# Optimization experiments

Hardware: AMD Instinct MI355X
Metric: run time of the kernel (lower is better)

## Reference

```python
import jax, jax.numpy as jnp
import numpy as np

B, N, C, H = 2, 2048, 1024, 16
HD = C // H  # head dim = 64


def setup_inputs() -> dict:
    key = jax.random.key(0)
    kq, kk, kv, km = jax.random.split(key, 4)
    q = jax.random.normal(kq, (B, N, C), dtype=jnp.float32)
    k = jax.random.normal(kk, (B, N, C), dtype=jnp.float32)
    v = jax.random.normal(kv, (B, N, C), dtype=jnp.float32)
    mask = jax.random.randint(km, (B, 1, N, N), 0, 2, dtype=jnp.int32)
    return {"q": q, "k": k, "v": v, "mask": mask}


def reference(q, k, v, mask):
    b, n, c = q.shape
    # (B, N, C) -> (B, H, N, HD)
    qh = q.reshape(b, n, H, HD).transpose(0, 2, 1, 3)
    kh = k.reshape(b, n, H, HD).transpose(0, 2, 1, 3)
    vh = v.reshape(b, n, H, HD).transpose(0, 2, 1, 3)
    scale = 1.0 / jnp.sqrt(jnp.float32(HD))
    # scores: (B, H, N, N)
    scores = jnp.einsum("bhqd,bhkd->bhqk", qh, kh) * scale
    scores = jnp.where(mask == 0, jnp.float32(-1e9), scores)
    probs = jax.nn.softmax(scores, axis=-1)
    atten = jnp.einsum("bhqk,bhkd->bhqd", probs, vh)
    # (B, H, N, HD) -> (B, N, C)
    return atten.transpose(0, 2, 1, 3).reshape(b, n, c)
```

## Files before the change

### kernel.cpp

```cpp
#include <hip/hip_runtime.h>
#include <hip/hip_bf16.h>

#define B_ 2
#define N_ 2048
#define C_ 1024
#define H_ 16
#define HD_ 64

#define KT 64
#define NT (N_ / KT)
#define TILE_E 4096
#define PSTR 72
#define NW 8
#define QB 128

#define NWM 4
#define QBM 64

typedef short s16x8 __attribute__((ext_vector_type(8)));
typedef short s16x4 __attribute__((ext_vector_type(4)));
typedef float f32x4 __attribute__((ext_vector_type(4)));

__device__ __forceinline__ ushort f2bf(float x) {
    __hip_bfloat16 h = __float2bfloat16(x);
    return *reinterpret_cast<ushort*>(&h);
}

__device__ __forceinline__ s16x8 cvt8(float4 a, float4 b) {
    union { s16x8 v; __hip_bfloat162 h[4]; } u;
    u.h[0] = __float22bfloat162_rn(float2{a.x, a.y});
    u.h[1] = __float22bfloat162_rn(float2{a.z, a.w});
    u.h[2] = __float22bfloat162_rn(float2{b.x, b.y});
    u.h[3] = __float22bfloat162_rn(float2{b.z, b.w});
    return u.v;
}

__device__ __forceinline__ void gll16(const void* g, void* l) {
    __builtin_amdgcn_global_load_lds(
        (const __attribute__((address_space(1))) unsigned*)g,
        (__attribute__((address_space(3))) unsigned*)l, 16, 0, 0);
}

__global__ __launch_bounds__(256)
void pack_mask(const int* __restrict__ M, unsigned long long* __restrict__ bits) {
    const int gw   = (blockIdx.x * 256 + threadIdx.x) >> 6;
    const int lane = threadIdx.x & 63;
#pragma unroll
    for (int it = 0; it < 16; ++it) {
        const size_t wi = (size_t)gw * 16 + it;
        unsigned long long bal = __ballot(M[wi * 64 + lane] != 0);
        if (lane == 0) bits[wi] = bal;
    }
}

__global__ __launch_bounds__(256)
void prepass(const int* __restrict__ M, const float* __restrict__ K,
             const float* __restrict__ V, unsigned long long* __restrict__ bits,
             ushort* __restrict__ Kw, ushort* __restrict__ Vw) {
    const int bid = blockIdx.x;
    const int tid = threadIdx.x;
    if (bid < 2048) {
        const int gw   = (bid * 256 + tid) >> 6;
        const int lane = tid & 63;
#pragma unroll
        for (int it = 0; it < 16; ++it) {
            const size_t wi = (size_t)gw * 16 + it;
            unsigned long long bal = __ballot(M[wi * 64 + lane] != 0);
            if (lane == 0) bits[wi] = bal;
        }
    } else if (bid < 4096) {
        const int gt = (bid - 2048) * 256 + tid;
        const int b  = gt >> 18;
        const int h  = (gt >> 14) & 15;
        const int n  = (gt >> 3) & 2047;
        const int db = gt & 7;
        const size_t src = (size_t)(b * N_ + n) * C_ + h * 64 + db * 8;
        float4 f0 = *(const float4*)(K + src);
        float4 f1 = *(const float4*)(K + src + 4);
        const int key = n & 63, kt = n >> 6;
        ushort* dst = Kw + (size_t)((b * H_ + h) * NT + kt) * TILE_E
                         + key * 64 + ((db ^ (key & 7)) * 8);
        *(s16x8*)dst = cvt8(f0, f1);
    } else {
        const int gt  = (bid - 4096) * 256 + tid;
        const int b   = gt >> 16;
        const int h   = (gt >> 12) & 15;
        const int kt  = (gt >> 7) & 31;
        const int kb4 = (gt >> 3) & 15;
        const int db  = gt & 7;
        const int key0 = kb4 * 4;
        float f[4][8];
#pragma unroll
        for (int i = 0; i < 4; ++i) {
            const size_t src = (size_t)(b * N_ + kt * 64 + key0 + i) * C_ + h * 64 + db * 8;
            *(float4*)&f[i][0] = *(const float4*)(V + src);
            *(float4*)&f[i][4] = *(const float4*)(V + src + 4);
        }
        ushort* tb = Vw + (size_t)((b * H_ + h) * NT + kt) * TILE_E;
#pragma unroll
        for (int j = 0; j < 8; ++j) {
            const int d = db * 8 + j;
            union { s16x4 v; __hip_bfloat162 h2[2]; } u;
            u.h2[0] = __float22bfloat162_rn(float2{f[0][j], f[1][j]});
            u.h2[1] = __float22bfloat162_rn(float2{f[2][j], f[3][j]});
            *(s16x4*)(tb + d * 64 + (((key0 >> 3) ^ (d & 7)) * 8) + (key0 & 7)) = u.v;
        }
    }
}

__global__ __launch_bounds__(256, 4)
void mha_fwd(const float* __restrict__ Q, const ushort* __restrict__ Kw,
             const ushort* __restrict__ Vw, const unsigned* __restrict__ bits,
             float* __restrict__ O) {
    __shared__ ushort Kl[2][TILE_E];
    __shared__ ushort Vt[2][TILE_E];
    __shared__ ushort Pl[NWM][16 * 64];

    const int sid = blockIdx.x;
    const int jj  = sid >> 3;
    const int hb  = ((sid & 7) << 2) | (jj & 3);
    const int qt  = jj >> 2;
    const int h   = hb & 15;
    const int b   = hb >> 4;

    const int tid  = threadIdx.x;
    const int w    = tid >> 6;
    const int lane = tid & 63;
    const int l16  = lane & 15;
    const int quad = lane >> 4;

    const size_t head_off = (size_t)b * N_ * C_ + (size_t)h * HD_;
    const int qb = qt * QBM + w * 16;

    const float qs = 0.125f * 1.44269504088896f;
    const size_t qoff = head_off + (size_t)(qb + l16) * C_ + quad * 8;
    float4 q0 = *(const float4*)(Q + qoff);
    float4 q1 = *(const float4*)(Q + qoff + 4);
    float4 q2 = *(const float4*)(Q + qoff + 32);
    float4 q3 = *(const float4*)(Q + qoff + 36);
    q0.x*=qs; q0.y*=qs; q0.z*=qs; q0.w*=qs;
    q1.x*=qs; q1.y*=qs; q1.z*=qs; q1.w*=qs;
    q2.x*=qs; q2.y*=qs; q2.z*=qs; q2.w*=qs;
    q3.x*=qs; q3.y*=qs; q3.z*=qs; q3.w*=qs;
    const s16x8 qa0 = cvt8(q0, q1);
    const s16x8 qa1 = cvt8(q2, q3);

    f32x4 acc[4];
#pragma unroll
    for (int c = 0; c < 4; ++c) acc[c] = f32x4{0.f, 0.f, 0.f, 0.f};
    float2 ls2 = {0.f, 0.f};

    const int fbase = l16 * 64 + ((quad ^ (l16 & 7)) * 8);
    const int prow  = l16 * 64;
    const int pswz  = (l16 & 7) << 1;

    const size_t tilebase = (size_t)((b * H_ + h) * NT) * TILE_E;
    const ushort* Kg = Kw + tilebase + (size_t)tid * 8;
    const ushort* Vg = Vw + tilebase + (size_t)tid * 8;

    const unsigned* mq = bits + ((size_t)b * N_ + qb + l16) * (N_ / 32);

    gll16(Kg,        &Kl[0][w * 512]);
    gll16(Kg + 2048, &Kl[0][w * 512 + 2048]);
    gll16(Vg,        &Vt[0][w * 512]);
    gll16(Vg + 2048, &Vt[0][w * 512 + 2048]);
    const ushort* Kg_pf = Kg + TILE_E;
    const ushort* Vg_pf = Vg + TILE_E;

    uint4 mw = *(const uint4*)mq;  mq += 4;

    for (int kt2 = 0; kt2 < NT; kt2 += 2) {
        const uint4 mw_nxt = *(const uint4*)mq;  mq += 4;
        const bool pf1 = (kt2 + 2 < NT);
#pragma unroll
        for (int u = 0; u < 2; ++u) {
            __syncthreads();
            if (u == 0 || pf1) {
                gll16(Kg_pf,        &Kl[1 - u][w * 512]);
                gll16(Kg_pf + 2048, &Kl[1 - u][w * 512 + 2048]);
                gll16(Vg_pf,        &Vt[1 - u][w * 512]);
                gll16(Vg_pf + 2048, &Vt[1 - u][w * 512 + 2048]);
                Kg_pf += TILE_E;  Vg_pf += TILE_E;
            }
            const unsigned w0 = u ? mw.z : mw.x;
            const unsigned w1 = u ? mw.w : mw.y;

            f32x4 s[4];
            __builtin_amdgcn_s_setprio(1);
#pragma unroll
            for (int t = 0; t < 4; ++t) {
                s16x8 kb0 = *(const s16x8*)(&Kl[u][fbase + t * 1024]);
                s16x8 kb1 = *(const s16x8*)(&Kl[u][(fbase ^ 32) + t * 1024]);
                f32x4 z = {0.f, 0.f, 0.f, 0.f};
                z = __builtin_amdgcn_mfma_f32_16x16x32_bf16(kb0, qa0, z, 0, 0, 0);
                z = __builtin_amdgcn_mfma_f32_16x16x32_bf16(kb1, qa1, z, 0, 0, 0);
                s[t] = z;
            }
            __builtin_amdgcn_s_setprio(0);

            const unsigned a0 = w0 >> (quad * 4);
            const unsigned a1 = w1 >> (quad * 4);
#pragma unroll
            for (int t = 0; t < 4; ++t) {
                const unsigned aw = (t < 2) ? a0 : a1;
                const int sh = (t & 1) * 16;
                float p0 = __builtin_amdgcn_exp2f(((aw >> (sh + 0)) & 1u) ? s[t][0] : -1e9f);
                float p1 = __builtin_amdgcn_exp2f(((aw >> (sh + 1)) & 1u) ? s[t][1] : -1e9f);
                float p2 = __builtin_amdgcn_exp2f(((aw >> (sh + 2)) & 1u) ? s[t][2] : -1e9f);
                float p3 = __builtin_amdgcn_exp2f(((aw >> (sh + 3)) & 1u) ? s[t][3] : -1e9f);
                ls2.x += p0 + p2;
                ls2.y += p1 + p3;
                union { s16x4 v; __hip_bfloat162 h2[2]; } uu;
                uu.h2[0] = __float22bfloat162_rn(float2{p0, p1});
                uu.h2[1] = __float22bfloat162_rn(float2{p2, p3});
                *(s16x4*)(&Pl[w][prow + ((((t << 2) | quad) ^ pswz) << 2)]) = uu.v;
            }

            __builtin_amdgcn_s_setprio(1);
#pragma unroll
            for (int half = 0; half < 2; ++half) {
                s16x8 pa = *(const s16x8*)(
                    &Pl[w][prow + ((((half << 3) | (quad << 1)) ^ pswz) << 2)]);
#pragma unroll
                for (int c = 0; c < 4; ++c) {
                    const int vidx = (half ? (fbase ^ 32) : fbase) + c * 1024;
                    s16x8 vb = *(const s16x8*)(&Vt[u][vidx]);
                    acc[c] = __builtin_amdgcn_mfma_f32_16x16x32_bf16(pa, vb, acc[c], 0, 0, 0);
                }
            }
            __builtin_amdgcn_s_setprio(0);
        }
        mw = mw_nxt;
    }

    float lsum = ls2.x + ls2.y;
    lsum += __shfl_xor(lsum, 16);
    lsum += __shfl_xor(lsum, 32);

#pragma unroll
    for (int r = 0; r < 4; ++r) {
        const float inv = 1.0f / __shfl(lsum, quad * 4 + r);
        const size_t obase = head_off + (size_t)(qb + quad * 4 + r) * C_;
        O[obase + l16]      = acc[0][r] * inv;
        O[obase + l16 + 16] = acc[1][r] * inv;
        O[obase + l16 + 32] = acc[2][r] * inv;
        O[obase + l16 + 48] = acc[3][r] * inv;
    }
}

#define KSTR 72
#define VSTR 72
__global__ __launch_bounds__(512, 4)
void mha_fwd_fb(const float* __restrict__ Q, const float* __restrict__ K,
                const float* __restrict__ V, const unsigned* __restrict__ bits,
                float* __restrict__ O) {
    __shared__ ushort Kl[2][KT * KSTR];
    __shared__ ushort Vt[2][HD_ * VSTR];
    __shared__ ushort Pl[NW][16 * PSTR];
    const int qt = blockIdx.x, h = blockIdx.y, b = blockIdx.z, tid = threadIdx.x;
    const int w = tid >> 6, lane = tid & 63, l16 = lane & 15, quad = lane >> 4;
    const size_t head_off = (size_t)b * N_ * C_ + (size_t)h * HD_;
    const int qb = qt * QB + w * 16;
    const float qs = 0.125f * 1.44269504088896f;
    const size_t qoff = head_off + (size_t)(qb + l16) * C_ + quad * 8;
    float4 q0 = *(const float4*)(Q + qoff);
    float4 q1 = *(const float4*)(Q + qoff + 4);
    float4 q2 = *(const float4*)(Q + qoff + 32);
    float4 q3 = *(const float4*)(Q + qoff + 36);
    q0.x*=qs; q0.y*=qs; q0.z*=qs; q0.w*=qs;
    q1.x*=qs; q1.y*=qs; q1.z*=qs; q1.w*=qs;
    q2.x*=qs; q2.y*=qs; q2.z*=qs; q2.w*=qs;
    q3.x*=qs; q3.y*=qs; q3.z*=qs; q3.w*=qs;
    const s16x8 qa0 = cvt8(q0, q1);
    const s16x8 qa1 = cvt8(q2, q3);
    f32x4 acc[4];
#pragma unroll
    for (int c = 0; c < 4; ++c) acc[c] = f32x4{0.f, 0.f, 0.f, 0.f};
    float lsum = 0.f;
    const int skey = tid >> 3, sd0 = (tid & 7) * 8;
    const int kp = tid >> 4, vd0 = (tid & 15) * 4;
    const int vcol = 2 * (kp & 3) + ((((kp >> 2) ^ (vd0 >> 3)) & 7) << 3);
    const unsigned* brow = bits + ((size_t)b * N_ + qb + l16) * (N_ / 32);
    const float SHIFT = 16.0f;
    {
        const size_t kbase = head_off + (size_t)skey * C_ + sd0;
        float4 kA = *(const float4*)(K + kbase);
        float4 kB = *(const float4*)(K + kbase + 4);
        *(s16x8*)(&Kl[0][skey * KSTR + sd0]) = cvt8(kA, kB);
        const size_t vbase = head_off + (size_t)(2 * kp) * C_ + vd0;
        float4 vA = *(const float4*)(V + vbase);
        float4 vB = *(const float4*)(V + vbase + C_);
        const float* ap = (const float*)&vA;
        const float* bp = (const float*)&vB;
#pragma unroll
        for (int i = 0; i < 4; ++i) {
            __hip_bfloat162 pr = __float22bfloat162_rn(float2{ap[i], bp[i]});
            *(unsigned*)(&Vt[0][(vd0 + i) * VSTR + vcol]) = *(unsigned*)&pr;
        }
    }
    for (int kt = 0; kt < NT; ++kt) {
        const int cur = kt & 1;
        float4 kA, kB, vA, vB;
        const bool has_next = (kt + 1 < NT);
        if (has_next) {
            const size_t kbase = head_off + (size_t)((kt + 1) * KT + skey) * C_ + sd0;
            kA = *(const float4*)(K + kbase);
            kB = *(const float4*)(K + kbase + 4);
            const size_t vbase = head_off + (size_t)((kt + 1) * KT + 2 * kp) * C_ + vd0;
            vA = *(const float4*)(V + vbase);
            vB = *(const float4*)(V + vbase + C_);
        }
        const unsigned w0 = brow[2 * kt];
        const unsigned w1 = brow[2 * kt + 1];
        __syncthreads();
        f32x4 s[4];
#pragma unroll
        for (int t = 0; t < 4; ++t) {
            s16x8 kb0 = *(const s16x8*)(&Kl[cur][(t * 16 + l16) * KSTR + quad * 8]);
            s16x8 kb1 = *(const s16x8*)(&Kl[cur][(t * 16 + l16) * KSTR + quad * 8 + 32]);
            f32x4 z = {0.f, 0.f, 0.f, 0.f};
            z = __builtin_amdgcn_mfma_f32_16x16x32_bf16(kb0, qa0, z, 0, 0, 0);
            z = __builtin_amdgcn_mfma_f32_16x16x32_bf16(kb1, qa1, z, 0, 0, 0);
            s[t] = z;
        }
        const unsigned a0 = w0 >> (quad * 4);
        const unsigned a1 = w1 >> (quad * 4);
#pragma unroll
        for (int t = 0; t < 4; ++t) {
            const unsigned aw = (t < 2) ? a0 : a1;
            const int sh = (t & 1) * 16;
            float p0 = exp2f((((aw >> (sh + 0)) & 1u) ? s[t][0] : -1e9f) - SHIFT);
            float p1 = exp2f((((aw >> (sh + 1)) & 1u) ? s[t][1] : -1e9f) - SHIFT);
            float p2 = exp2f((((aw >> (sh + 2)) & 1u) ? s[t][2] : -1e9f) - SHIFT);
            float p3 = exp2f((((aw >> (sh + 3)) & 1u) ? s[t][3] : -1e9f) - SHIFT);
            lsum += (p0 + p1) + (p2 + p3);
            union { s16x4 v; __hip_bfloat162 h2[2]; } uu;
            uu.h2[0] = __float22bfloat162_rn(float2{p0, p1});
            uu.h2[1] = __float22bfloat162_rn(float2{p2, p3});
            *(s16x4*)(&Pl[w][l16 * PSTR + t * 16 + quad * 4]) = uu.v;
        }
#pragma unroll
        for (int half = 0; half < 2; ++half) {
            s16x8 pa = *(const s16x8*)(&Pl[w][l16 * PSTR + half * 32 + quad * 8]);
#pragma unroll
            for (int c = 0; c < 4; ++c) {
                const int dr = c * 16 + l16;
                const int blk = (half * 4 + quad) ^ ((dr >> 3) & 7);
                s16x8 vb = *(const s16x8*)(&Vt[cur][dr * VSTR + blk * 8]);
                acc[c] = __builtin_amdgcn_mfma_f32_16x16x32_bf16(pa, vb, acc[c], 0, 0, 0);
            }
        }
        if (has_next) {
            *(s16x8*)(&Kl[1 - cur][skey * KSTR + sd0]) = cvt8(kA, kB);
            const float* ap = (const float*)&vA;
            const float* bp = (const float*)&vB;
#pragma unroll
            for (int i = 0; i < 4; ++i) {
                __hip_bfloat162 pr = __float22bfloat162_rn(float2{ap[i], bp[i]});
                *(unsigned*)(&Vt[1 - cur][(vd0 + i) * VSTR + vcol]) = *(unsigned*)&pr;
            }
        }
    }
    lsum += __shfl_xor(lsum, 16);
    lsum += __shfl_xor(lsum, 32);
#pragma unroll
    for (int r = 0; r < 4; ++r) {
        const float inv = 1.0f / __shfl(lsum, quad * 4 + r);
        const size_t obase = head_off + (size_t)(qb + quad * 4 + r) * C_;
        O[obase + l16]      = acc[0][r] * inv;
        O[obase + l16 + 16] = acc[1][r] * inv;
        O[obase + l16 + 32] = acc[2][r] * inv;
        O[obase + l16 + 48] = acc[3][r] * inv;
    }
}

extern "C" void kernel_launch(void* const* d_in, const int* in_sizes, int n_in,
                              void* d_out, int out_size, void* d_ws, size_t ws_size,
                              hipStream_t stream) {
    const float* q = (const float*)d_in[0];
    const float* k = (const float*)d_in[1];
    const float* v = (const float*)d_in[2];
    const int*   m = (const int*)d_in[3];
    float*       o = (float*)d_out;

    const size_t BITS_BYTES = (size_t)B_ * N_ * N_ / 8;
    const size_t KV_BYTES   = (size_t)B_ * H_ * N_ * HD_ * 2;
    const size_t NEED       = BITS_BYTES + 2 * KV_BYTES;

    unsigned long long* bits = (unsigned long long*)d_ws;

    if (ws_size >= NEED) {
        ushort* kw = (ushort*)((char*)d_ws + BITS_BYTES);
        ushort* vw = (ushort*)((char*)d_ws + BITS_BYTES + KV_BYTES);
        hipLaunchKernelGGL(prepass, dim3(4608), dim3(256), 0, stream,
                           m, k, v, bits, kw, vw);
        hipLaunchKernelGGL(mha_fwd, dim3(1024), dim3(256), 0, stream,
                           q, kw, vw, (const unsigned*)bits, o);
    } else {
        hipLaunchKernelGGL(pack_mask, dim3(2048), dim3(256), 0, stream, m, bits);
        dim3 grid(N_ / QB, H_, B_);
        hipLaunchKernelGGL(mha_fwd_fb, grid, dim3(512), 0, stream,
                           q, k, v, (const unsigned*)bits, o);
    }
}
```

Before: 174.1 us.

## Process two 16-row query tiles per wave and compute row sums via MFMA

Each wave in the main attention kernel now handles 32 query rows (two 16-row tiles) instead of 16, with 2 waves per block instead of 4. Each K/V fragment read from LDS is reused across both tiles, and the softmax denominators are accumulated with an extra MFMA against a ones vector instead of scalar adds and shuffles. The mask-packing prepass is also rewritten to have each thread read int4 vectors and build 16 bits directly instead of using wave ballots. The change raises register pressure and halves the threads available to issue each tile's global-to-LDS loads, and the bf16-rounded probabilities now feed the denominator.

```diff
diff --git a/kernel.cpp b/kernel.cpp
--- a/kernel.cpp
+++ b/kernel.cpp
@@ -14,17 +14,12 @@
 #define NW 8
 #define QB 128
 
-#define NWM 4
+#define NWM 2
 #define QBM 64
 
 typedef short s16x8 __attribute__((ext_vector_type(8)));
 typedef short s16x4 __attribute__((ext_vector_type(4)));
 typedef float f32x4 __attribute__((ext_vector_type(4)));
-
-__device__ __forceinline__ ushort f2bf(float x) {
-    __hip_bfloat16 h = __float2bfloat16(x);
-    return *reinterpret_cast<ushort*>(&h);
-}
 
 __device__ __forceinline__ s16x8 cvt8(float4 a, float4 b) {
     union { s16x8 v; __hip_bfloat162 h[4]; } u;
@@ -60,14 +55,18 @@
     const int bid = blockIdx.x;
     const int tid = threadIdx.x;
     if (bid < 2048) {
-        const int gw   = (bid * 256 + tid) >> 6;
-        const int lane = tid & 63;
-#pragma unroll
-        for (int it = 0; it < 16; ++it) {
-            const size_t wi = (size_t)gw * 16 + it;
-            unsigned long long bal = __ballot(M[wi * 64 + lane] != 0);
-            if (lane == 0) bits[wi] = bal;
-        }
+        const int gt = bid * 256 + tid;
+        const int4* src = (const int4*)M + (size_t)gt * 4;
+        unsigned r = 0;
+#pragma unroll
+        for (int c = 0; c < 4; ++c) {
+            const int4 m4 = src[c];
+            r |= (m4.x != 0 ? 1u : 0u) << (c * 4 + 0);
+            r |= (m4.y != 0 ? 1u : 0u) << (c * 4 + 1);
+            r |= (m4.z != 0 ? 1u : 0u) << (c * 4 + 2);
+            r |= (m4.w != 0 ? 1u : 0u) << (c * 4 + 3);
+        }
+        ((ushort*)bits)[gt] = (ushort)r;
     } else if (bid < 4096) {
         const int gt = (bid - 2048) * 256 + tid;
         const int b  = gt >> 18;
@@ -108,13 +107,13 @@
     }
 }
 
-__global__ __launch_bounds__(256, 4)
+__global__ __launch_bounds__(128, 2)
 void mha_fwd(const float* __restrict__ Q, const ushort* __restrict__ Kw,
              const ushort* __restrict__ Vw, const unsigned* __restrict__ bits,
              float* __restrict__ O) {
     __shared__ ushort Kl[2][TILE_E];
     __shared__ ushort Vt[2][TILE_E];
-    __shared__ ushort Pl[NWM][16 * 64];
+    __shared__ ushort Pl[NWM][2][16 * 64];
 
     const int sid = blockIdx.x;
     const int jj  = sid >> 3;
@@ -130,25 +129,40 @@
     const int quad = lane >> 4;
 
     const size_t head_off = (size_t)b * N_ * C_ + (size_t)h * HD_;
-    const int qb = qt * QBM + w * 16;
+    const int qb = qt * QBM + w * 32;
 
     const float qs = 0.125f * 1.44269504088896f;
-    const size_t qoff = head_off + (size_t)(qb + l16) * C_ + quad * 8;
-    float4 q0 = *(const float4*)(Q + qoff);
-    float4 q1 = *(const float4*)(Q + qoff + 4);
-    float4 q2 = *(const float4*)(Q + qoff + 32);
-    float4 q3 = *(const float4*)(Q + qoff + 36);
+    const size_t qoffA = head_off + (size_t)(qb + l16) * C_ + quad * 8;
+    const size_t qoffB = head_off + (size_t)(qb + 16 + l16) * C_ + quad * 8;
+    float4 q0 = *(const float4*)(Q + qoffA);
+    float4 q1 = *(const float4*)(Q + qoffA + 4);
+    float4 q2 = *(const float4*)(Q + qoffA + 32);
+    float4 q3 = *(const float4*)(Q + qoffA + 36);
+    float4 q4 = *(const float4*)(Q + qoffB);
+    float4 q5 = *(const float4*)(Q + qoffB + 4);
+    float4 q6 = *(const float4*)(Q + qoffB + 32);
+    float4 q7 = *(const float4*)(Q + qoffB + 36);
     q0.x*=qs; q0.y*=qs; q0.z*=qs; q0.w*=qs;
     q1.x*=qs; q1.y*=qs; q1.z*=qs; q1.w*=qs;
     q2.x*=qs; q2.y*=qs; q2.z*=qs; q2.w*=qs;
     q3.x*=qs; q3.y*=qs; q3.z*=qs; q3.w*=qs;
+    q4.x*=qs; q4.y*=qs; q4.z*=qs; q4.w*=qs;
+    q5.x*=qs; q5.y*=qs; q5.z*=qs; q5.w*=qs;
+    q6.x*=qs; q6.y*=qs; q6.z*=qs; q6.w*=qs;
+    q7.x*=qs; q7.y*=qs; q7.z*=qs; q7.w*=qs;
     const s16x8 qa0 = cvt8(q0, q1);
     const s16x8 qa1 = cvt8(q2, q3);
-
-    f32x4 acc[4];
-#pragma unroll
-    for (int c = 0; c < 4; ++c) acc[c] = f32x4{0.f, 0.f, 0.f, 0.f};
-    float2 ls2 = {0.f, 0.f};
+    const s16x8 qa2 = cvt8(q4, q5);
+    const s16x8 qa3 = cvt8(q6, q7);
+
+    s16x8 onesb;
+#pragma unroll
+    for (int i = 0; i < 8; ++i) onesb[i] = (short)0x3F80;
+
+    f32x4 accA[4], accB[4], sumA, sumB;
+#pragma unroll
+    for (int c = 0; c < 4; ++c) { accA[c] = f32x4{0,0,0,0}; accB[c] = f32x4{0,0,0,0}; }
+    sumA = f32x4{0,0,0,0};  sumB = f32x4{0,0,0,0};
 
     const int fbase = l16 * 64 + ((quad ^ (l16 & 7)) * 8);
     const int prow  = l16 * 64;
@@ -158,93 +172,130 @@
     const ushort* Kg = Kw + tilebase + (size_t)tid * 8;
     const ushort* Vg = Vw + tilebase + (size_t)tid * 8;
 
-    const unsigned* mq = bits + ((size_t)b * N_ + qb + l16) * (N_ / 32);
-
-    gll16(Kg,        &Kl[0][w * 512]);
-    gll16(Kg + 2048, &Kl[0][w * 512 + 2048]);
-    gll16(Vg,        &Vt[0][w * 512]);
-    gll16(Vg + 2048, &Vt[0][w * 512 + 2048]);
+    const unsigned* mqA = bits + ((size_t)b * N_ + qb + l16) * (N_ / 32);
+    const unsigned* mqB = mqA + 16 * (N_ / 32);
+
+#pragma unroll
+    for (int c = 0; c < 4; ++c) {
+        gll16(Kg + c * 1024, &Kl[0][w * 512 + c * 1024]);
+        gll16(Vg + c * 1024, &Vt[0][w * 512 + c * 1024]);
+    }
     const ushort* Kg_pf = Kg + TILE_E;
     const ushort* Vg_pf = Vg + TILE_E;
 
-    uint4 mw = *(const uint4*)mq;  mq += 4;
+    uint4 mwA = *(const uint4*)mqA;  mqA += 4;
+    uint4 mwB = *(const uint4*)mqB;  mqB += 4;
 
     for (int kt2 = 0; kt2 < NT; kt2 += 2) {
-        const uint4 mw_nxt = *(const uint4*)mq;  mq += 4;
+        const uint4 mwA_n = *(const uint4*)mqA;  mqA += 4;
+        const uint4 mwB_n = *(const uint4*)mqB;  mqB += 4;
         const bool pf1 = (kt2 + 2 < NT);
 #pragma unroll
         for (int u = 0; u < 2; ++u) {
             __syncthreads();
             if (u == 0 || pf1) {
-                gll16(Kg_pf,        &Kl[1 - u][w * 512]);
-                gll16(Kg_pf + 2048, &Kl[1 - u][w * 512 + 2048]);
-                gll16(Vg_pf,        &Vt[1 - u][w * 512]);
-                gll16(Vg_pf + 2048, &Vt[1 - u][w * 512 + 2048]);
+#pragma unroll
+                for (int c = 0; c < 4; ++c) {
+                    gll16(Kg_pf + c * 1024, &Kl[1 - u][w * 512 + c * 1024]);
+                    gll16(Vg_pf + c * 1024, &Vt[1 - u][w * 512 + c * 1024]);
+                }
                 Kg_pf += TILE_E;  Vg_pf += TILE_E;
             }
-            const unsigned w0 = u ? mw.z : mw.x;
-            const unsigned w1 = u ? mw.w : mw.y;
-
-            f32x4 s[4];
+            const unsigned wA0 = u ? mwA.z : mwA.x;
+            const unsigned wA1 = u ? mwA.w : mwA.y;
+            const unsigned wB0 = u ? mwB.z : mwB.x;
+            const unsigned wB1 = u ? mwB.w : mwB.y;
+
+            f32x4 sA[4], sB[4];
             __builtin_amdgcn_s_setprio(1);
 #pragma unroll
             for (int t = 0; t < 4; ++t) {
                 s16x8 kb0 = *(const s16x8*)(&Kl[u][fbase + t * 1024]);
                 s16x8 kb1 = *(const s16x8*)(&Kl[u][(fbase ^ 32) + t * 1024]);
-                f32x4 z = {0.f, 0.f, 0.f, 0.f};
-                z = __builtin_amdgcn_mfma_f32_16x16x32_bf16(kb0, qa0, z, 0, 0, 0);
-                z = __builtin_amdgcn_mfma_f32_16x16x32_bf16(kb1, qa1, z, 0, 0, 0);
-                s[t] = z;
+                f32x4 zA = {0.f,0.f,0.f,0.f}, zB = {0.f,0.f,0.f,0.f};
+                zA = __builtin_amdgcn_mfma_f32_16x16x32_bf16(kb0, qa0, zA, 0, 0, 0);
+                zA = __builtin_amdgcn_mfma_f32_16x16x32_bf16(kb1, qa1, zA, 0, 0, 0);
+                zB = __builtin_amdgcn_mfma_f32_16x16x32_bf16(kb0, qa2, zB, 0, 0, 0);
+                zB = __builtin_amdgcn_mfma_f32_16x16x32_bf16(kb1, qa3, zB, 0, 0, 0);
+                sA[t] = zA;  sB[t] = zB;
             }
             __builtin_amdgcn_s_setprio(0);
 
-            const unsigned a0 = w0 >> (quad * 4);
-            const unsigned a1 = w1 >> (quad * 4);
+            const unsigned aA0 = wA0 >> (quad * 4);
+            const unsigned aA1 = wA1 >> (quad * 4);
 #pragma unroll
             for (int t = 0; t < 4; ++t) {
-                const unsigned aw = (t < 2) ? a0 : a1;
+                const unsigned aw = (t < 2) ? aA0 : aA1;
                 const int sh = (t & 1) * 16;
-                float p0 = __builtin_amdgcn_exp2f(((aw >> (sh + 0)) & 1u) ? s[t][0] : -1e9f);
-                float p1 = __builtin_amdgcn_exp2f(((aw >> (sh + 1)) & 1u) ? s[t][1] : -1e9f);
-                float p2 = __builtin_amdgcn_exp2f(((aw >> (sh + 2)) & 1u) ? s[t][2] : -1e9f);
-                float p3 = __builtin_amdgcn_exp2f(((aw >> (sh + 3)) & 1u) ? s[t][3] : -1e9f);
-                ls2.x += p0 + p2;
-                ls2.y += p1 + p3;
+                float p0 = __builtin_amdgcn_exp2f(((aw >> (sh + 0)) & 1u) ? sA[t][0] : -1e9f);
+                float p1 = __builtin_amdgcn_exp2f(((aw >> (sh + 1)) & 1u) ? sA[t][1] : -1e9f);
+                float p2 = __builtin_amdgcn_exp2f(((aw >> (sh + 2)) & 1u) ? sA[t][2] : -1e9f);
+                float p3 = __builtin_amdgcn_exp2f(((aw >> (sh + 3)) & 1u) ? sA[t][3] : -1e9f);
                 union { s16x4 v; __hip_bfloat162 h2[2]; } uu;
                 uu.h2[0] = __float22bfloat162_rn(float2{p0, p1});
                 uu.h2[1] = __float22bfloat162_rn(float2{p2, p3});
-                *(s16x4*)(&Pl[w][prow + ((((t << 2) | quad) ^ pswz) << 2)]) = uu.v;
+                *(s16x4*)(&Pl[w][0][prow + ((((t << 2) | quad) ^ pswz) << 2)]) = uu.v;
+            }
+            const unsigned aB0 = wB0 >> (quad * 4);
+            const unsigned aB1 = wB1 >> (quad * 4);
+#pragma unroll
+            for (int t = 0; t < 4; ++t) {
+                const unsigned aw = (t < 2) ? aB0 : aB1;
+                const int sh = (t & 1) * 16;
+                float p0 = __builtin_amdgcn_exp2f(((aw >> (sh + 0)) & 1u) ? sB[t][0] : -1e9f);
+                float p1 = __builtin_amdgcn_exp2f(((aw >> (sh + 1)) & 1u) ? sB[t][1] : -1e9f);
+                float p2 = __builtin_amdgcn_exp2f(((aw >> (sh + 2)) & 1u) ? sB[t][2] : -1e9f);
+                float p3 = __builtin_amdgcn_exp2f(((aw >> (sh + 3)) & 1u) ? sB[t][3] : -1e9f);
+                union { s16x4 v; __hip_bfloat162 h2[2]; } uu;
+                uu.h2[0] = __float22bfloat162_rn(float2{p0, p1});
+                uu.h2[1] = __float22bfloat162_rn(float2{p2, p3});
+                *(s16x4*)(&Pl[w][1][prow + ((((t << 2) | quad) ^ pswz) << 2)]) = uu.v;
             }
 
             __builtin_amdgcn_s_setprio(1);
 #pragma unroll
             for (int half = 0; half < 2; ++half) {
                 s16x8 pa = *(const s16x8*)(
-                    &Pl[w][prow + ((((half << 3) | (quad << 1)) ^ pswz) << 2)]);
+                    &Pl[w][0][prow + ((((half << 3) | (quad << 1)) ^ pswz) << 2)]);
 #pragma unroll
                 for (int c = 0; c < 4; ++c) {
                     const int vidx = (half ? (fbase ^ 32) : fbase) + c * 1024;
                     s16x8 vb = *(const s16x8*)(&Vt[u][vidx]);
-                    acc[c] = __builtin_amdgcn_mfma_f32_16x16x32_bf16(pa, vb, acc[c], 0, 0, 0);
+                    accA[c] = __builtin_amdgcn_mfma_f32_16x16x32_bf16(pa, vb, accA[c], 0, 0, 0);
                 }
+                sumA = __builtin_amdgcn_mfma_f32_16x16x32_bf16(pa, onesb, sumA, 0, 0, 0);
+            }
+#pragma unroll
+            for (int half = 0; half < 2; ++half) {
+                s16x8 pa = *(const s16x8*)(
+                    &Pl[w][1][prow + ((((half << 3) | (quad << 1)) ^ pswz) << 2)]);
+#pragma unroll
+                for (int c = 0; c < 4; ++c) {
+                    const int vidx = (half ? (fbase ^ 32) : fbase) + c * 1024;
+                    s16x8 vb = *(const s16x8*)(&Vt[u][vidx]);
+                    accB[c] = __builtin_amdgcn_mfma_f32_16x16x32_bf16(pa, vb, accB[c], 0, 0, 0);
+                }
+                sumB = __builtin_amdgcn_mfma_f32_16x16x32_bf16(pa, onesb, sumB, 0, 0, 0);
             }
             __builtin_amdgcn_s_setprio(0);
         }
-        mw = mw_nxt;
-    }
-
-    float lsum = ls2.x + ls2.y;
-    lsum += __shfl_xor(lsum, 16);
-    lsum += __shfl_xor(lsum, 32);
+        mwA = mwA_n;  mwB = mwB_n;
+    }
 
 #pragma unroll
     for (int r = 0; r < 4; ++r) {
-        const float inv = 1.0f / __shfl(lsum, quad * 4 + r);
-        const size_t obase = head_off + (size_t)(qb + quad * 4 + r) * C_;
-        O[obase + l16]      = acc[0][r] * inv;
-        O[obase + l16 + 16] = acc[1][r] * inv;
-        O[obase + l16 + 32] = acc[2][r] * inv;
-        O[obase + l16 + 48] = acc[3][r] * inv;
+        const float invA = 1.0f / sumA[r];
+        const size_t oA = head_off + (size_t)(qb + quad * 4 + r) * C_;
+        O[oA + l16]      = accA[0][r] * invA;
+        O[oA + l16 + 16] = accA[1][r] * invA;
+        O[oA + l16 + 32] = accA[2][r] * invA;
+        O[oA + l16 + 48] = accA[3][r] * invA;
+        const float invB = 1.0f / sumB[r];
+        const size_t oB = head_off + (size_t)(qb + 16 + quad * 4 + r) * C_;
+        O[oB + l16]      = accB[0][r] * invB;
+        O[oB + l16 + 16] = accB[1][r] * invB;
+        O[oB + l16 + 32] = accB[2][r] * invB;
+        O[oB + l16 + 48] = accB[3][r] * invB;
     }
 }
 
@@ -394,7 +445,7 @@
         ushort* vw = (ushort*)((char*)d_ws + BITS_BYTES + KV_BYTES);
         hipLaunchKernelGGL(prepass, dim3(4608), dim3(256), 0, stream,
                            m, k, v, bits, kw, vw);
-        hipLaunchKernelGGL(mha_fwd, dim3(1024), dim3(256), 0, stream,
+        hipLaunchKernelGGL(mha_fwd, dim3(1024), dim3(128), 0, stream,
                            q, kw, vw, (const unsigned*)bits, o);
     } else {
         hipLaunchKernelGGL(pack_mask, dim3(2048), dim3(256), 0, stream, m, bits);
```

New measurement: 173.8 us. Within noise of the previous version (-0.2%).

## Keep softmax probabilities in registers via permuted K layout and MFMA row sums

Applied to the files above, without the earlier changes.

Permutes the key order inside each K tile during the prepass so that the S=K·Q MFMA output registers already match the A-operand layout of the P·V MFMA. This removes the per-wave LDS round trip for P (the store and reload through Pl) and changes how the mask bits are read to follow the permuted key order. Row sums now come from an extra MFMA against a ones vector instead of scalar adds and cross-lane shuffles. The mask packing is also rewritten to use vectorized int4 loads that produce 16-bit words. The cost is one additional MFMA per half-tile, and the sums are now accumulated from bf16-rounded probabilities.

```diff
diff --git a/kernel.cpp b/kernel.cpp
--- a/kernel.cpp
+++ b/kernel.cpp
@@ -20,11 +20,6 @@
 typedef short s16x8 __attribute__((ext_vector_type(8)));
 typedef short s16x4 __attribute__((ext_vector_type(4)));
 typedef float f32x4 __attribute__((ext_vector_type(4)));
-
-__device__ __forceinline__ ushort f2bf(float x) {
-    __hip_bfloat16 h = __float2bfloat16(x);
-    return *reinterpret_cast<ushort*>(&h);
-}
 
 __device__ __forceinline__ s16x8 cvt8(float4 a, float4 b) {
     union { s16x8 v; __hip_bfloat162 h[4]; } u;
@@ -60,14 +55,18 @@
     const int bid = blockIdx.x;
     const int tid = threadIdx.x;
     if (bid < 2048) {
-        const int gw   = (bid * 256 + tid) >> 6;
-        const int lane = tid & 63;
-#pragma unroll
-        for (int it = 0; it < 16; ++it) {
-            const size_t wi = (size_t)gw * 16 + it;
-            unsigned long long bal = __ballot(M[wi * 64 + lane] != 0);
-            if (lane == 0) bits[wi] = bal;
-        }
+        const int gt = bid * 256 + tid;
+        const int4* src = (const int4*)M + (size_t)gt * 4;
+        unsigned r = 0;
+#pragma unroll
+        for (int c = 0; c < 4; ++c) {
+            const int4 m4 = src[c];
+            r |= (m4.x != 0 ? 1u : 0u) << (c * 4 + 0);
+            r |= (m4.y != 0 ? 1u : 0u) << (c * 4 + 1);
+            r |= (m4.z != 0 ? 1u : 0u) << (c * 4 + 2);
+            r |= (m4.w != 0 ? 1u : 0u) << (c * 4 + 3);
+        }
+        ((ushort*)bits)[gt] = (ushort)r;
     } else if (bid < 4096) {
         const int gt = (bid - 2048) * 256 + tid;
         const int b  = gt >> 18;
@@ -78,8 +77,9 @@
         float4 f0 = *(const float4*)(K + src);
         float4 f1 = *(const float4*)(K + src + 4);
         const int key = n & 63, kt = n >> 6;
+        const int p = (key & 32) | ((key & 4) << 2) | ((key >> 1) & 12) | (key & 3);
         ushort* dst = Kw + (size_t)((b * H_ + h) * NT + kt) * TILE_E
-                         + key * 64 + ((db ^ (key & 7)) * 8);
+                         + p * 64 + ((db ^ (p & 7)) * 8);
         *(s16x8*)dst = cvt8(f0, f1);
     } else {
         const int gt  = (bid - 4096) * 256 + tid;
@@ -114,7 +114,6 @@
              float* __restrict__ O) {
     __shared__ ushort Kl[2][TILE_E];
     __shared__ ushort Vt[2][TILE_E];
-    __shared__ ushort Pl[NWM][16 * 64];
 
     const int sid = blockIdx.x;
     const int jj  = sid >> 3;
@@ -145,14 +144,16 @@
     const s16x8 qa0 = cvt8(q0, q1);
     const s16x8 qa1 = cvt8(q2, q3);
 
+    s16x8 onesb;
+#pragma unroll
+    for (int i = 0; i < 8; ++i) onesb[i] = (short)0x3F80;
+
     f32x4 acc[4];
 #pragma unroll
     for (int c = 0; c < 4; ++c) acc[c] = f32x4{0.f, 0.f, 0.f, 0.f};
-    float2 ls2 = {0.f, 0.f};
+    f32x4 sum = f32x4{0.f, 0.f, 0.f, 0.f};
 
     const int fbase = l16 * 64 + ((quad ^ (l16 & 7)) * 8);
-    const int prow  = l16 * 64;
-    const int pswz  = (l16 & 7) << 1;
 
     const size_t tilebase = (size_t)((b * H_ + h) * NT) * TILE_E;
     const ushort* Kg = Kw + tilebase + (size_t)tid * 8;
@@ -198,48 +199,44 @@
             }
             __builtin_amdgcn_s_setprio(0);
 
-            const unsigned a0 = w0 >> (quad * 4);
-            const unsigned a1 = w1 >> (quad * 4);
+            const unsigned aw0 = w0 >> (quad * 8);
+            const unsigned aw1 = w1 >> (quad * 8);
+            union { s16x8 v; __hip_bfloat162 h2[4]; } pk0, pk1;
 #pragma unroll
             for (int t = 0; t < 4; ++t) {
-                const unsigned aw = (t < 2) ? a0 : a1;
-                const int sh = (t & 1) * 16;
-                float p0 = __builtin_amdgcn_exp2f(((aw >> (sh + 0)) & 1u) ? s[t][0] : -1e9f);
-                float p1 = __builtin_amdgcn_exp2f(((aw >> (sh + 1)) & 1u) ? s[t][1] : -1e9f);
-                float p2 = __builtin_amdgcn_exp2f(((aw >> (sh + 2)) & 1u) ? s[t][2] : -1e9f);
-                float p3 = __builtin_amdgcn_exp2f(((aw >> (sh + 3)) & 1u) ? s[t][3] : -1e9f);
-                ls2.x += p0 + p2;
-                ls2.y += p1 + p3;
-                union { s16x4 v; __hip_bfloat162 h2[2]; } uu;
-                uu.h2[0] = __float22bfloat162_rn(float2{p0, p1});
-                uu.h2[1] = __float22bfloat162_rn(float2{p2, p3});
-                *(s16x4*)(&Pl[w][prow + ((((t << 2) | quad) ^ pswz) << 2)]) = uu.v;
+                const unsigned aw = ((t < 2) ? aw0 : aw1) >> ((t & 1) * 4);
+                float p0 = __builtin_amdgcn_exp2f(((aw >> 0) & 1u) ? s[t][0] : -1e9f);
+                float p1 = __builtin_amdgcn_exp2f(((aw >> 1) & 1u) ? s[t][1] : -1e9f);
+                float p2 = __builtin_amdgcn_exp2f(((aw >> 2) & 1u) ? s[t][2] : -1e9f);
+                float p3 = __builtin_amdgcn_exp2f(((aw >> 3) & 1u) ? s[t][3] : -1e9f);
+                __hip_bfloat162 lo = __float22bfloat162_rn(float2{p0, p1});
+                __hip_bfloat162 hi = __float22bfloat162_rn(float2{p2, p3});
+                if      (t == 0) { pk0.h2[0] = lo; pk0.h2[1] = hi; }
+                else if (t == 1) { pk0.h2[2] = lo; pk0.h2[3] = hi; }
+                else if (t == 2) { pk1.h2[0] = lo; pk1.h2[1] = hi; }
+                else             { pk1.h2[2] = lo; pk1.h2[3] = hi; }
             }
 
             __builtin_amdgcn_s_setprio(1);
 #pragma unroll
             for (int half = 0; half < 2; ++half) {
-                s16x8 pa = *(const s16x8*)(
-                    &Pl[w][prow + ((((half << 3) | (quad << 1)) ^ pswz) << 2)]);
+                const s16x8 pa = half ? pk1.v : pk0.v;
 #pragma unroll
                 for (int c = 0; c < 4; ++c) {
                     const int vidx = (half ? (fbase ^ 32) : fbase) + c * 1024;
                     s16x8 vb = *(const s16x8*)(&Vt[u][vidx]);
                     acc[c] = __builtin_amdgcn_mfma_f32_16x16x32_bf16(pa, vb, acc[c], 0, 0, 0);
                 }
+                sum = __builtin_amdgcn_mfma_f32_16x16x32_bf16(pa, onesb, sum, 0, 0, 0);
             }
             __builtin_amdgcn_s_setprio(0);
         }
         mw = mw_nxt;
     }
 
-    float lsum = ls2.x + ls2.y;
-    lsum += __shfl_xor(lsum, 16);
-    lsum += __shfl_xor(lsum, 32);
-
 #pragma unroll
     for (int r = 0; r < 4; ++r) {
-        const float inv = 1.0f / __shfl(lsum, quad * 4 + r);
+        const float inv = 1.0f / sum[r];
         const size_t obase = head_off + (size_t)(qb + quad * 4 + r) * C_;
         O[obase + l16]      = acc[0][r] * inv;
         O[obase + l16 + 16] = acc[1][r] * inv;
```

Result: faster. 165.7 us (-4.8%).
